# Performance work log

Measured on AMD Instinct MI355X. Metric: run time of the kernel, lower is better.

Reference implementation:

```python
import jax, jax.numpy as jnp
import numpy as np

N, IN_CAPS, OUT_CAPS, IN_LEN, OUT_LEN = 64, 256, 128, 16, 32
NUM_ITERATIONS = 3


def _squash(t, axis=-1):
    # scale * t / sqrt(||t||^2) with scale = ||t||^2 / (1 + ||t||^2)
    sq = jnp.sum(t * t, axis=axis, keepdims=True)
    return (sq / (1.0 + sq)) * t / jnp.sqrt(sq)


def setup_inputs() -> dict:
    key = jax.random.key(0)
    k1, k2 = jax.random.split(key)
    x = jax.random.normal(k1, (N, IN_CAPS, IN_LEN), dtype=jnp.float32)
    weight = jax.random.normal(k2, (OUT_CAPS, IN_CAPS, IN_LEN, OUT_LEN), dtype=jnp.float32)
    return {"x": x, "weight": weight}


def reference(x, weight):
    # priors: [out_caps, N, in_caps, out_len]  (torch keeps an extra singleton dim)
    priors = jnp.einsum('nik,oikl->onil', x, weight)
    logits = jnp.zeros_like(priors)
    outputs = None
    for i in range(NUM_ITERATIONS):
        # torch softmax(dim=2) == softmax over the in_caps axis
        probs = jax.nn.softmax(logits, axis=2)
        s = jnp.sum(probs * priors, axis=2, keepdims=True)  # [O, N, 1, L]
        outputs = _squash(s, axis=-1)
        if i != NUM_ITERATIONS - 1:
            # delta broadcasts over out_len, as in the torch code
            logits = logits + jnp.sum(priors * outputs, axis=-1, keepdims=True)
    # squeeze routing dim, transpose to [N, out_caps, out_len]
    return jnp.transpose(outputs[:, :, 0, :], (1, 0, 2))
```

## Files before the change

### kernel.cpp

```cpp
#include <hip/hip_runtime.h>


#define ICAPS 256
#define OCAPS 128
#define WS_XC 67108864ull
#define WS_NEED 68157440ull
#define KPAD 20
#define SLABW 1408

typedef __attribute__((ext_vector_type(8))) short s16x8;
typedef __attribute__((ext_vector_type(16))) float f32x16;

union u4s8 { unsigned u[4]; s16x8 v; };

__device__ inline unsigned rne_adj(unsigned u) {
    return u + 0x7FFFu + ((u >> 16) & 1u);
}

__device__ inline void split8(const float* f, s16x8& hi, s16x8& lo) {
    u4s8 H, L;
    #pragma unroll
    for (int c = 0; c < 4; ++c) {
        const unsigned u0 = __float_as_uint(f[2 * c]);
        const unsigned u1 = __float_as_uint(f[2 * c + 1]);
        const unsigned r0 = rne_adj(u0), r1 = rne_adj(u1);
        H.u[c] = __builtin_amdgcn_perm(r1, r0, 0x07060302u);
        const float h0 = __uint_as_float(r0 & 0xFFFF0000u);
        const float h1 = __uint_as_float(r1 & 0xFFFF0000u);
        const unsigned l0 = rne_adj(__float_as_uint(f[2 * c] - h0));
        const unsigned l1 = rne_adj(__float_as_uint(f[2 * c + 1] - h1));
        L.u[c] = __builtin_amdgcn_perm(l1, l0, 0x07060302u);
    }
    hi = H.v; lo = L.v;
}

__global__ __launch_bounds__(512)
void caps_prep(const float* __restrict__ x, const float* __restrict__ w,
               unsigned char* __restrict__ ws) {
    __shared__ float T[8][32 * KPAD];
    const int wv = threadIdx.x >> 6, lane = threadIdx.x & 63;
    const int gid = blockIdx.x * 8 + wv;
    float f[8];
    s16x8 hi, lo;

    if (gid < 32768) {
        const float* src = w + (size_t)gid * 512 + lane * 8;
        const float4 a = *(const float4*)src;
        const float4 b = *(const float4*)(src + 4);
        const float v[8] = {a.x, a.y, a.z, a.w, b.x, b.y, b.z, b.w};
        {
            float* Tw = &T[wv][0];
            const int k = lane >> 2, l0 = (lane & 3) * 8;
            #pragma unroll
            for (int j = 0; j < 8; ++j) Tw[(l0 + j) * KPAD + k] = v[j];
        }
        asm volatile("s_waitcnt lgkmcnt(0)" ::: "memory");
        {
            const float* rd = &T[wv][(lane & 31) * KPAD + (lane >> 5) * 8];
            const float4 ra = *(const float4*)rd;
            const float4 rb = *(const float4*)(rd + 4);
            f[0] = ra.x; f[1] = ra.y; f[2] = ra.z; f[3] = ra.w;
            f[4] = rb.x; f[5] = rb.y; f[6] = rb.z; f[7] = rb.w;
        }
        split8(f, hi, lo);
        s16x8* WC = (s16x8*)ws;
        WC[(size_t)gid * 128 + lane] = hi;
        WC[(size_t)gid * 128 + 64 + lane] = lo;
    } else if (gid < 33280) {
        const int id = gid - 32768;
        const int nh = id >> 8, i = id & 255;
        const int n = lane & 31, kb = (lane >> 5) * 8;
        const float* src = x + ((size_t)(nh * 32 + n) * ICAPS + i) * 16 + kb;
        const float4 a = *(const float4*)src;
        const float4 b = *(const float4*)(src + 4);
        f[0] = a.x; f[1] = a.y; f[2] = a.z; f[3] = a.w;
        f[4] = b.x; f[5] = b.y; f[6] = b.z; f[7] = b.w;
        split8(f, hi, lo);
        s16x8* XC = (s16x8*)(ws + WS_XC);
        XC[(size_t)id * 128 + lane] = hi;
        XC[(size_t)id * 128 + 64 + lane] = lo;
    }
}


#define MF(a, b, c) __builtin_amdgcn_mfma_f32_32x32x16_bf16(a, b, c, 0, 0, 0)

#define LD1(N, ii)                                   \
    {                                                \
        const size_t b_ = (size_t)(ii) * 128;        \
        N##0 = Wp[b_]; N##1 = Wp[b_ + 64];           \
        N##2 = Xp[b_]; N##3 = Xp[b_ + 64];           \
    }

#define TRIP(N, ACC)                 \
    {                                \
        ACC = MF(N##1, N##2, ACC);   \
        ACC = MF(N##0, N##3, ACC);   \
        ACC = MF(N##0, N##2, ACC);   \
    }

#define SOFTSTEP(P, ii)                                                   \
    {                                                                     \
        float da = P[0] * vr[0], db = P[8] * vr[8];                       \
        _Pragma("unroll")                                                 \
        for (int r = 1; r < 8; ++r) {                                     \
            da = fmaf(P[r], vr[r], da);                                   \
            db = fmaf(P[r + 8], vr[r + 8], db);                           \
        }                                                                 \
        float d = da + db;                                                \
        d += __shfl_xor(d, 32);                     \
        if (pass == 1) {                                                  \
            if (half == 0) lg[(ii) * 32 + n] = d;                         \
        } else {                                                          \
            d += lg[(ii) * 32 + n];                                       \
        }                                                                 \
        const float e = __expf(d);                                        \
        z += e;                                                           \
        _Pragma("unroll")                                                 \
        for (int r = 0; r < 16; ++r) uacc[r] = fmaf(e, P[r], uacc[r]);    \
    }

#define PROC1(N, ii)                 \
    {                                \
        f32x16 P = {};               \
        TRIP(N, P);                  \
        SOFTSTEP(P, ii);             \
    }

__global__ __launch_bounds__(512, 1)
void caps_main(const unsigned char* __restrict__ ws, float* __restrict__ out) {
    __shared__ float lg[ICAPS * 32];
    __shared__ float slab[8 * SLABW];
    __shared__ float svv[32 * 33];
    __shared__ float zz[8 * 32];
    __shared__ float zinv[32];

    const int t = threadIdx.x, wv = t >> 6, lane = t & 63;
    const int o = blockIdx.x & 127, nh = blockIdx.x >> 7;
    const int n = lane & 31, half = lane >> 5;

    const s16x8* Wp = (const s16x8*)ws + (size_t)o * ICAPS * 128 + lane;
    const s16x8* Xp = (const s16x8*)(ws + WS_XC) + (size_t)nh * ICAPS * 128 + lane;

    float vr[16];
    const int ibase = wv * 32;

    s16x8 FA0, FA1, FA2, FA3;
    s16x8 FB0, FB1, FB2, FB3;
    s16x8 FC0, FC1, FC2, FC3;

    LD1(FA, ibase + 0);
    LD1(FB, ibase + 1);
    LD1(FC, ibase + 2);

    for (int pass = 0; pass < 3; ++pass) {
        float uacc[16];
        #pragma unroll
        for (int r = 0; r < 16; ++r) uacc[r] = 0.f;
        float z = 0.f;

        if (pass == 0) {
            f32x16 Pa = {}, Pb = {}, Pc = {};
            #pragma unroll 1
            for (int g = 0; g < 9; ++g) {
                const int s0 = ibase + 3 * g;
                TRIP(FA, Pa); LD1(FA, s0 + 3);
                TRIP(FB, Pb); LD1(FB, s0 + 4);
                TRIP(FC, Pc); LD1(FC, s0 + 5);
            }
            TRIP(FA, Pa); LD1(FA, ibase + 30);
            TRIP(FB, Pb); LD1(FB, ibase + 31);
            TRIP(FC, Pc);
            TRIP(FA, Pa);
            TRIP(FB, Pb);
            #pragma unroll
            for (int r = 0; r < 16; ++r) uacc[r] = (Pa[r] + Pb[r]) + Pc[r];
        } else {
            #pragma unroll 1
            for (int g = 0; g < 9; ++g) {
                const int s0 = ibase + 3 * g;
                PROC1(FA, s0 + 0); LD1(FA, s0 + 3);
                PROC1(FB, s0 + 1); LD1(FB, s0 + 4);
                PROC1(FC, s0 + 2); LD1(FC, s0 + 5);
            }
            PROC1(FA, ibase + 27); LD1(FA, ibase + 30);
            PROC1(FB, ibase + 28); LD1(FB, ibase + 31);
            PROC1(FC, ibase + 29);
            PROC1(FA, ibase + 30);
            PROC1(FB, ibase + 31);
        }

        if (pass < 2) {
            LD1(FA, ibase + 0);
            LD1(FB, ibase + 1);
            LD1(FC, ibase + 2);
        }

        #pragma unroll
        for (int c = 0; c < 4; ++c)
            *(float4*)(&slab[wv * SLABW + lane * 20 + c * 4]) =
                make_float4(uacc[4 * c], uacc[4 * c + 1], uacc[4 * c + 2], uacc[4 * c + 3]);
        if (pass > 0 && half == 0) zz[wv * 32 + n] = z;
        __syncthreads();

        #pragma unroll
        for (int hh = 0; hh < 2; ++hh) {
            const int e = t + hh * 512;
            const int lw = e >> 4, r = e & 15;
            float s = 0.f;
            #pragma unroll
            for (int w8 = 0; w8 < 8; ++w8) s += slab[w8 * SLABW + lw * 20 + r];
            const int nn = lw & 31, ll = (r & 3) + 8 * (r >> 2) + 4 * (lw >> 5);
            svv[nn * 33 + ll] = s;
        }
        if (t < 32) {
            if (pass == 0) zinv[t] = 1.0f / 256.0f;
            else {
                float zs = 0.f;
                #pragma unroll
                for (int w8 = 0; w8 < 8; ++w8) zs += zz[w8 * 32 + t];
                zinv[t] = 1.0f / zs;
            }
        }
        __syncthreads();

        {
            const int nq = t >> 4, sub = t & 15;
            const float a = svv[nq * 33 + sub] * zinv[nq];
            const float b = svv[nq * 33 + sub + 16] * zinv[nq];
            float sq = a * a + b * b;
            #pragma unroll
            for (int m = 1; m < 16; m <<= 1) sq += __shfl_xor(sq, m, 16);
            const float sc = sqrtf(sq) / (1.0f + sq);
            if (pass == 2) {
                const int ng = nh * 32 + nq;
                out[((size_t)ng * OCAPS + o) * 32 + sub] = a * sc;
                out[((size_t)ng * OCAPS + o) * 32 + sub + 16] = b * sc;
            } else {
                svv[nq * 33 + sub] = a * sc;
                svv[nq * 33 + sub + 16] = b * sc;
            }
        }
        if (pass < 2) {
            __syncthreads();
            #pragma unroll
            for (int r = 0; r < 16; ++r) {
                const int l = (r & 3) + 8 * (r >> 2) + 4 * half;
                vr[r] = svv[n * 33 + l];
            }
        }
    }
}

#define KLEN  16
#define LLEN  32
#define TN    16
#define LGS   257
#define XROW  20
#define XIST  (TN * XROW + 4)
#define SVS   33
#define RBS   33
#define NSTG  32
#define NSTEP (ICAPS / NSTG)

__global__ __launch_bounds__(512, 2)
void caps_route_fb(const float* __restrict__ xg_all,
                   const float* __restrict__ wg_all,
                   float* __restrict__ out) {
    __shared__ float lg[TN * LGS];
    __shared__ float xt[NSTG * XIST];
    __shared__ float sv[TN * SVS];
    __shared__ float zz[8][TN];
    __shared__ float zinv[TN];

    const int t   = threadIdx.x;
    const int o   = blockIdx.x & 127;
    const int n0  = (blockIdx.x >> 7) * TN;
    const int isp = t >> 4;
    const int lb  = (t >> 2) & 3;
    const int nb  = t & 3;
    const int l0  = lb * 8;

    const float* xg = xg_all + (size_t)n0 * ICAPS * KLEN;
    const float* wg = wg_all + (size_t)o * ICAPS * KLEN * LLEN;

    for (int pass = 0; pass < 3; ++pass) {
        float u[4][8];
        float zq[4] = {0.f, 0.f, 0.f, 0.f};
        #pragma unroll
        for (int q = 0; q < 4; ++q)
            #pragma unroll
            for (int r = 0; r < 8; ++r) u[q][r] = 0.f;

        for (int st = 0; st < NSTEP; ++st) {
            const int i0 = st * NSTG;
            __syncthreads();
            #pragma unroll
            for (int j = 0; j < 4; ++j) {
                const int g   = j * 512 + t;
                const int nn  = g >> 7;
                const int rem = g & 127;
                const int il  = rem >> 2;
                const int k4c = rem & 3;
                *(float4*)(&xt[il * XIST + nn * XROW + k4c * 4]) =
                    *(const float4*)(xg + (size_t)(nn * ICAPS + i0 + il) * KLEN + k4c * 4);
            }
            __syncthreads();

            const int i = i0 + isp;
            const float* wp = wg + (size_t)i * (KLEN * LLEN) + l0;
            const float* xp = &xt[isp * XIST];
            float P[4][8];
            #pragma unroll
            for (int q = 0; q < 4; ++q)
                #pragma unroll
                for (int r = 0; r < 8; ++r) P[q][r] = 0.f;

            #pragma unroll
            for (int k4 = 0; k4 < 4; ++k4) {
                float xq[4][4];
                #pragma unroll
                for (int q = 0; q < 4; ++q)
                    *(float4*)(&xq[q][0]) = *(const float4*)(xp + (nb + 4 * q) * XROW + k4 * 4);
                #pragma unroll
                for (int kk = 0; kk < 4; ++kk) {
                    const int k = k4 * 4 + kk;
                    const float4 wa = *(const float4*)(wp + k * LLEN);
                    const float4 wb = *(const float4*)(wp + k * LLEN + 4);
                    #pragma unroll
                    for (int q = 0; q < 4; ++q) {
                        const float xv = xq[q][kk];
                        P[q][0] = fmaf(xv, wa.x, P[q][0]);
                        P[q][1] = fmaf(xv, wa.y, P[q][1]);
                        P[q][2] = fmaf(xv, wa.z, P[q][2]);
                        P[q][3] = fmaf(xv, wa.w, P[q][3]);
                        P[q][4] = fmaf(xv, wb.x, P[q][4]);
                        P[q][5] = fmaf(xv, wb.y, P[q][5]);
                        P[q][6] = fmaf(xv, wb.z, P[q][6]);
                        P[q][7] = fmaf(xv, wb.w, P[q][7]);
                    }
                }
            }

            if (pass == 0) {
                #pragma unroll
                for (int q = 0; q < 4; ++q)
                    #pragma unroll
                    for (int r = 0; r < 8; ++r) u[q][r] += P[q][r];
            } else {
                #pragma unroll
                for (int q = 0; q < 4; ++q) {
                    const float* vp = &sv[(nb + 4 * q) * SVS + l0];
                    float d = P[q][0] * vp[0] + P[q][1] * vp[1] + P[q][2] * vp[2] + P[q][3] * vp[3]
                            + P[q][4] * vp[4] + P[q][5] * vp[5] + P[q][6] * vp[6] + P[q][7] * vp[7];
                    d += __shfl_xor(d, 4);
                    d += __shfl_xor(d, 8);
                    float lnew = d;
                    if (pass == 2) lnew += lg[(nb + 4 * q) * LGS + i];
                    else if (lb == 0) lg[(nb + 4 * q) * LGS + i] = lnew;
                    const float e = __expf(lnew);
                    zq[q] += e;
                    #pragma unroll
                    for (int r = 0; r < 8; ++r) u[q][r] = fmaf(e, P[q][r], u[q][r]);
                }
            }
        }

        #pragma unroll
        for (int q = 0; q < 4; ++q) {
            #pragma unroll
            for (int r = 0; r < 8; ++r) {
                float v = u[q][r];
                v += __shfl_xor(v, 16);
                v += __shfl_xor(v, 32);
                u[q][r] = v;
            }
            float zv = zq[q];
            zv += __shfl_xor(zv, 16);
            zv += __shfl_xor(zv, 32);
            zq[q] = zv;
        }
        __syncthreads();
        {
            const int wvv = t >> 6, lane = t & 63;
            if (lane < 16) {
                float* rb = &xt[wvv * (16 * RBS) + lane * RBS];
                #pragma unroll
                for (int q = 0; q < 4; ++q)
                    #pragma unroll
                    for (int r = 0; r < 8; ++r) rb[q * 8 + r] = u[q][r];
            }
            if (pass > 0 && lane < 4) {
                #pragma unroll
                for (int q = 0; q < 4; ++q) zz[wvv][lane + 4 * q] = zq[q];
            }
        }
        __syncthreads();
        {
            const int low4 = t >> 5, qr = t & 31;
            const int qq = qr >> 3, rr = qr & 7;
            const int lbb = low4 >> 2, nbb = low4 & 3;
            float ssum = 0.f;
            #pragma unroll
            for (int w8 = 0; w8 < 8; ++w8) ssum += xt[w8 * (16 * RBS) + low4 * RBS + qr];
            sv[(nbb + 4 * qq) * SVS + lbb * 8 + rr] = ssum;
        }
        if (t < TN) {
            if (pass == 0) zinv[t] = 1.0f / 256.0f;
            else {
                float zs = 0.f;
                #pragma unroll
                for (int w8 = 0; w8 < 8; ++w8) zs += zz[w8][t];
                zinv[t] = 1.0f / zs;
            }
        }
        __syncthreads();
        {
            const int nn = t >> 5, l = t & 31;
            const float val = sv[nn * SVS + l] * zinv[nn];
            float sq = val * val;
            #pragma unroll
            for (int m = 1; m < 32; m <<= 1) sq += __shfl_xor(sq, m, 32);
            const float sc = sqrtf(sq) / (1.0f + sq);
            if (pass == 2)
                out[((size_t)(n0 + nn) * OCAPS + o) * LLEN + l] = val * sc;
            else
                sv[nn * SVS + l] = val * sc;
        }
    }
}

extern "C" void kernel_launch(void* const* d_in, const int* in_sizes, int n_in,
                              void* d_out, int out_size, void* d_ws, size_t ws_size,
                              hipStream_t stream) {
    const float* x = (const float*)d_in[0];
    const float* w = (const float*)d_in[1];
    float* outp = (float*)d_out;
    if (ws_size >= WS_NEED) {
        caps_prep<<<dim3(4160), dim3(512), 0, stream>>>(x, w, (unsigned char*)d_ws);
        caps_main<<<dim3(256), dim3(512), 0, stream>>>((const unsigned char*)d_ws, outp);
    } else {
        caps_route_fb<<<dim3(512), dim3(512), 0, stream>>>(x, w, outp);
    }
}
```

Measured before the change: 150.0 us.

## Stage weight fragments through LDS via async global_load_lds with deeper pipeline

Weight fragments are no longer loaded into registers. They are copied asynchronously from global memory into a 4-slot LDS ring per wave using global_load_lds, with explicit vmcnt waits, then read back from LDS before the MFMAs. X fragments still go through registers but are prefetched two steps ahead. The aim is a deeper prefetch with lower register pressure, so more weight loads are in flight and the MFMA and softmax work hides more memory latency. The hand-tuned vmcnt counts are fragile, and the extra LDS traffic, roughly 64KB more shared memory, could cost performance.

```diff
diff --git a/kernel.cpp b/kernel.cpp
--- a/kernel.cpp
+++ b/kernel.cpp
@@ -85,51 +85,71 @@
 
 #define MF(a, b, c) __builtin_amdgcn_mfma_f32_32x32x16_bf16(a, b, c, 0, 0, 0)
 
-#define LD1(N, ii)                                   \
-    {                                                \
-        const size_t b_ = (size_t)(ii) * 128;        \
-        N##0 = Wp[b_]; N##1 = Wp[b_ + 64];           \
-        N##2 = Xp[b_]; N##3 = Xp[b_ + 64];           \
-    }
-
-#define TRIP(N, ACC)                 \
-    {                                \
-        ACC = MF(N##1, N##2, ACC);   \
-        ACC = MF(N##0, N##3, ACC);   \
-        ACC = MF(N##0, N##2, ACC);   \
-    }
-
-#define SOFTSTEP(P, ii)                                                   \
-    {                                                                     \
-        float da = P[0] * vr[0], db = P[8] * vr[8];                       \
-        _Pragma("unroll")                                                 \
-        for (int r = 1; r < 8; ++r) {                                     \
-            da = fmaf(P[r], vr[r], da);                                   \
-            db = fmaf(P[r + 8], vr[r + 8], db);                           \
-        }                                                                 \
-        float d = da + db;                                                \
-        d += __shfl_xor(d, 32);                     \
-        if (pass == 1) {                                                  \
-            if (half == 0) lg[(ii) * 32 + n] = d;                         \
-        } else {                                                          \
-            d += lg[(ii) * 32 + n];                                       \
-        }                                                                 \
-        const float e = __expf(d);                                        \
-        z += e;                                                           \
-        _Pragma("unroll")                                                 \
-        for (int r = 0; r < 16; ++r) uacc[r] = fmaf(e, P[r], uacc[r]);    \
-    }
-
-#define PROC1(N, ii)                 \
-    {                                \
-        f32x16 P = {};               \
-        TRIP(N, P);                  \
-        SOFTSTEP(P, ii);             \
+#define GLL(gp, lp) __builtin_amdgcn_global_load_lds(                       \
+        (const __attribute__((address_space(1))) void*)(gp),                \
+        (__attribute__((address_space(3))) void*)(lp), 16, 0, 0)
+
+#define STAGE(SL, ii)                                                       \
+    {                                                                       \
+        const s16x8* g_ = Wp + (size_t)(ii) * 128;                          \
+        GLL(g_,      &Wst[wv][SL][0]);                                      \
+        GLL(g_ + 64, &Wst[wv][SL][64]);                                     \
+    }
+
+#define LDX(N, ii)                                                          \
+    {                                                                       \
+        const size_t b_ = (size_t)(ii) * 128;                               \
+        N##h = Xp[b_]; N##l = Xp[b_ + 64];                                  \
+    }
+
+#define VMW_(N) asm volatile("s_waitcnt vmcnt(" #N ")" ::: "memory")
+#define VMW(N) { VMW_(N); __builtin_amdgcn_sched_barrier(0); }
+
+#define READW(SL)                                                           \
+    {                                                                       \
+        const s16x8* w_ = &Wst[wv][SL][0];                                  \
+        whi = w_[lane]; wlo = w_[lane + 64];                                \
+    }
+
+#define TRIPX(XN, ACC)                                                      \
+    {                                                                       \
+        ACC = MF(wlo, XN##h, ACC);                                          \
+        ACC = MF(whi, XN##l, ACC);                                          \
+        ACC = MF(whi, XN##h, ACC);                                          \
+    }
+
+#define SOFTSTEP(P, ii)                                                     \
+    {                                                                       \
+        float da = P[0] * vr[0], db = P[8] * vr[8];                         \
+        _Pragma("unroll")                                                   \
+        for (int r = 1; r < 8; ++r) {                                       \
+            da = fmaf(P[r], vr[r], da);                                     \
+            db = fmaf(P[r + 8], vr[r + 8], db);                             \
+        }                                                                   \
+        float d = da + db;                                                  \
+        d += __shfl_xor(d, 32);                       \
+        if (pass == 1) {                                                    \
+            if (half == 0) lg[(ii) * 32 + n] = d;                           \
+        } else {                                                            \
+            d += lg[(ii) * 32 + n];                                         \
+        }                                                                   \
+        const float e = __expf(d);                                          \
+        z += e;                                                             \
+        _Pragma("unroll")                                                   \
+        for (int r = 0; r < 16; ++r) uacc[r] = fmaf(e, P[r], uacc[r]);      \
+    }
+
+#define PROCX(XN, ii)                                                       \
+    {                                                                       \
+        f32x16 P = {};                                                      \
+        TRIPX(XN, P);                                                       \
+        SOFTSTEP(P, ii);                                                    \
     }
 
 __global__ __launch_bounds__(512, 1)
 void caps_main(const unsigned char* __restrict__ ws, float* __restrict__ out) {
     __shared__ float lg[ICAPS * 32];
+    __shared__ s16x8 Wst[8][4][128];
     __shared__ float slab[8 * SLABW];
     __shared__ float svv[32 * 33];
     __shared__ float zz[8 * 32];
@@ -145,13 +165,14 @@
     float vr[16];
     const int ibase = wv * 32;
 
-    s16x8 FA0, FA1, FA2, FA3;
-    s16x8 FB0, FB1, FB2, FB3;
-    s16x8 FC0, FC1, FC2, FC3;
-
-    LD1(FA, ibase + 0);
-    LD1(FB, ibase + 1);
-    LD1(FC, ibase + 2);
+    s16x8 whi, wlo;
+    s16x8 X0h, X0l, X1h, X1l, X2h, X2l, X3h, X3l;
+
+    STAGE(0, ibase + 0);
+    STAGE(1, ibase + 1);
+    STAGE(2, ibase + 2);
+    LDX(X0, ibase + 0);
+    LDX(X1, ibase + 1);
 
     for (int pass = 0; pass < 3; ++pass) {
         float uacc[16];
@@ -160,40 +181,50 @@
         float z = 0.f;
 
         if (pass == 0) {
-            f32x16 Pa = {}, Pb = {}, Pc = {};
+            f32x16 Pa = {}, Pb = {};
+            STAGE(3, ibase + 3); VMW(10); READW(0); LDX(X2, ibase + 2); TRIPX(X0, Pa);
+            STAGE(0, ibase + 4); VMW(12); READW(1); LDX(X3, ibase + 3); TRIPX(X1, Pb);
+            STAGE(1, ibase + 5); VMW(14); READW(2); LDX(X0, ibase + 4); TRIPX(X2, Pa);
             #pragma unroll 1
-            for (int g = 0; g < 9; ++g) {
-                const int s0 = ibase + 3 * g;
-                TRIP(FA, Pa); LD1(FA, s0 + 3);
-                TRIP(FB, Pb); LD1(FB, s0 + 4);
-                TRIP(FC, Pc); LD1(FC, s0 + 5);
-            }
-            TRIP(FA, Pa); LD1(FA, ibase + 30);
-            TRIP(FB, Pb); LD1(FB, ibase + 31);
-            TRIP(FC, Pc);
-            TRIP(FA, Pa);
-            TRIP(FB, Pb);
-            #pragma unroll
-            for (int r = 0; r < 16; ++r) uacc[r] = (Pa[r] + Pb[r]) + Pc[r];
+            for (int q = 0; q < 6; ++q) {
+                const int s0 = ibase + 3 + 4 * q;
+                STAGE(2, s0 + 3); VMW(12); READW(3); LDX(X1, s0 + 2); TRIPX(X3, Pb);
+                STAGE(3, s0 + 4); VMW(12); READW(0); LDX(X2, s0 + 3); TRIPX(X0, Pa);
+                STAGE(0, s0 + 5); VMW(12); READW(1); LDX(X3, s0 + 4); TRIPX(X1, Pb);
+                STAGE(1, s0 + 6); VMW(12); READW(2); LDX(X0, s0 + 5); TRIPX(X2, Pa);
+            }
+            STAGE(2, ibase + 30); VMW(12); READW(3); LDX(X1, ibase + 29); TRIPX(X3, Pb);
+            STAGE(3, ibase + 31); VMW(12); READW(0); LDX(X2, ibase + 30); TRIPX(X0, Pa);
+            VMW(10); READW(1); LDX(X3, ibase + 31); TRIPX(X1, Pb);
+            VMW(8);  READW(2); TRIPX(X2, Pa);
+            VMW(4);  READW(3); TRIPX(X3, Pb);
+            #pragma unroll
+            for (int r = 0; r < 16; ++r) uacc[r] = Pa[r] + Pb[r];
         } else {
+            STAGE(3, ibase + 3); VMW(10); READW(0); LDX(X2, ibase + 2); PROCX(X0, ibase + 0);
+            STAGE(0, ibase + 4); VMW(12); READW(1); LDX(X3, ibase + 3); PROCX(X1, ibase + 1);
+            STAGE(1, ibase + 5); VMW(14); READW(2); LDX(X0, ibase + 4); PROCX(X2, ibase + 2);
             #pragma unroll 1
-            for (int g = 0; g < 9; ++g) {
-                const int s0 = ibase + 3 * g;
-                PROC1(FA, s0 + 0); LD1(FA, s0 + 3);
-                PROC1(FB, s0 + 1); LD1(FB, s0 + 4);
-                PROC1(FC, s0 + 2); LD1(FC, s0 + 5);
-            }
-            PROC1(FA, ibase + 27); LD1(FA, ibase + 30);
-            PROC1(FB, ibase + 28); LD1(FB, ibase + 31);
-            PROC1(FC, ibase + 29);
-            PROC1(FA, ibase + 30);
-            PROC1(FB, ibase + 31);
+            for (int q = 0; q < 6; ++q) {
+                const int s0 = ibase + 3 + 4 * q;
+                STAGE(2, s0 + 3); VMW(12); READW(3); LDX(X1, s0 + 2); PROCX(X3, s0 + 0);
+                STAGE(3, s0 + 4); VMW(12); READW(0); LDX(X2, s0 + 3); PROCX(X0, s0 + 1);
+                STAGE(0, s0 + 5); VMW(12); READW(1); LDX(X3, s0 + 4); PROCX(X1, s0 + 2);
+                STAGE(1, s0 + 6); VMW(12); READW(2); LDX(X0, s0 + 5); PROCX(X2, s0 + 3);
+            }
+            STAGE(2, ibase + 30); VMW(12); READW(3); LDX(X1, ibase + 29); PROCX(X3, ibase + 27);
+            STAGE(3, ibase + 31); VMW(12); READW(0); LDX(X2, ibase + 30); PROCX(X0, ibase + 28);
+            VMW(10); READW(1); LDX(X3, ibase + 31); PROCX(X1, ibase + 29);
+            VMW(8);  READW(2); PROCX(X2, ibase + 30);
+            VMW(4);  READW(3); PROCX(X3, ibase + 31);
         }
 
         if (pass < 2) {
-            LD1(FA, ibase + 0);
-            LD1(FB, ibase + 1);
-            LD1(FC, ibase + 2);
+            STAGE(0, ibase + 0);
+            STAGE(1, ibase + 1);
+            STAGE(2, ibase + 2);
+            LDX(X0, ibase + 0);
+            LDX(X1, ibase + 1);
         }
 
         #pragma unroll
```

After: 150.7 us. No clear change (+0.5%).
